# Kernel optimization log

Hardware: AMD Instinct MI355X
Metric: run time of the kernel (lower is better)

Reference implementation:

```python
import jax, jax.numpy as jnp
import numpy as np

V = 50000      # nodes
E = 800000     # edges (avg degree 16)
H = 128        # hidden_nf
EA = 2         # edge_attr dim after concat with radial dist
NL = 2         # n_layers
NORM = 100.0   # normalization_factor (agg_method='sum')
NORM_CONST = 1.0


def setup_inputs() -> dict:
    key = jax.random.key(0)
    ks = jax.random.split(key, 24)
    f32 = jnp.float32
    def rn(k, shp, s=0.02):
        return jax.random.normal(k, shp, dtype=f32) * s
    return {
        "h": jax.random.normal(ks[0], (V, H), f32),
        "x": jax.random.normal(ks[1], (V, 3), f32),
        "edge_index": jax.random.randint(ks[2], (2, E), 0, V),
        "edge_attr": jax.random.normal(ks[3], (E, 1), f32),
        # GCL params, stacked over NL layers
        "ew1": rn(ks[4], (NL, 2 * H + EA, H)), "eb1": jnp.zeros((NL, H), f32),
        "ew2": rn(ks[5], (NL, H, H)),          "eb2": jnp.zeros((NL, H), f32),
        "aw":  rn(ks[6], (NL, H, 1)),          "ab":  jnp.zeros((NL, 1), f32),
        "nw1": rn(ks[7], (NL, 2 * H, H)),      "nb1": jnp.zeros((NL, H), f32),
        "nw2": rn(ks[8], (NL, H, H)),          "nb2": jnp.zeros((NL, H), f32),
        # EquivariantUpdate coord_mlp params
        "cw1": rn(ks[9], (2 * H + EA, H)),     "cb1": jnp.zeros((H,), f32),
        "cw2": rn(ks[10], (H, H)),             "cb2": jnp.zeros((H,), f32),
        "cw3": rn(ks[11], (H, 1), 0.001),      # xavier gain=0.001, no bias
    }


def reference(h, x, edge_index, edge_attr,
              ew1, eb1, ew2, eb2, aw, ab, nw1, nb1, nw2, nb2,
              cw1, cb1, cw2, cb2, cw3):
    silu = jax.nn.silu
    row, col = edge_index[0], edge_index[1]

    # coord2diff
    coord_diff = x[row] - x[col]                               # [E,3]
    radial = jnp.sum(coord_diff ** 2, axis=1, keepdims=True)   # [E,1]
    norm = jnp.sqrt(radial + 1e-8)
    coord_diff = coord_diff / (norm + NORM_CONST)

    ea = jnp.concatenate([radial, edge_attr], axis=1)          # [E,EA]

    # n_layers GCL blocks with attention, agg_method='sum'
    for i in range(NL):
        inp = jnp.concatenate([h[row], h[col], ea], axis=1)    # [E,2H+EA]
        mij = silu(inp @ ew1[i] + eb1[i])
        mij = silu(mij @ ew2[i] + eb2[i])                      # [E,H]
        att = jax.nn.sigmoid(mij @ aw[i] + ab[i])              # [E,1]
        edge_feat = mij * att
        agg = jax.ops.segment_sum(edge_feat, row, num_segments=V) / NORM  # [V,H]
        t = jnp.concatenate([h, agg], axis=1)                  # [V,2H]
        t = silu(t @ nw1[i] + nb1[i])
        h = h + (t @ nw2[i] + nb2[i])

    # EquivariantUpdate (tanh=False)
    inp = jnp.concatenate([h[row], h[col], ea], axis=1)        # [E,2H+EA]
    t = silu(inp @ cw1 + cb1)
    t = silu(t @ cw2 + cb2)
    s = t @ cw3                                                # [E,1]
    trans = coord_diff * s                                     # [E,3]
    aggc = jax.ops.segment_sum(trans, row, num_segments=V) / NORM
    x = x + aggc
    return (h, x)
```

## Files before the change

### kernel.cpp

```cpp
#include <hip/hip_runtime.h>

#define V_N 50000
#define E_N 800000
#define H_N 128

typedef __bf16 bf16;
typedef bf16 bf16x4 __attribute__((ext_vector_type(4)));
typedef bf16 bf16x8 __attribute__((ext_vector_type(8)));
typedef float f32x4 __attribute__((ext_vector_type(4)));

#define PQ_STRIDE 512

__device__ __forceinline__ float silu_f(float x) {
    return x * __builtin_amdgcn_rcpf(1.0f + __expf(-x));
}
__device__ __forceinline__ float sigmoid_f(float x) {
    return __builtin_amdgcn_rcpf(1.0f + __expf(-x));
}

__global__ void k_weights(const float* __restrict__ ew1, const float* __restrict__ ew2,
                          const float* __restrict__ nw1, const float* __restrict__ nw2,
                          const float* __restrict__ cw1, const float* __restrict__ cw2,
                          const float* __restrict__ eb1, const float* __restrict__ cb1,
                          bf16* __restrict__ projT, bf16* __restrict__ ew2T,
                          bf16* __restrict__ nw1T, bf16* __restrict__ nw2T,
                          bf16* __restrict__ cprojT, bf16* __restrict__ cw2T,
                          float* __restrict__ biasPQ, float* __restrict__ biasCPQ) {
    int idx = blockIdx.x * 256 + threadIdx.x;
    if (idx < 65536) {
        int l = idx >> 15, rem = idx & 32767;
        int n = rem >> 7, k = rem & 127;
        const float* W = ew1 + l * 258 * 128;
        projT[idx] = (bf16)((n < 128) ? W[k * 128 + n] : W[(128 + k) * 128 + (n - 128)]);
    } else if (idx < 98304) {
        int r = idx - 65536;
        int l = r >> 14, rem = r & 16383;
        int n = rem >> 7, k = rem & 127;
        ew2T[r] = (bf16)(ew2[l * 16384 + k * 128 + n]);
    } else if (idx < 163840) {
        int r = idx - 98304;
        int l = r >> 15, rem = r & 32767;
        int n = rem >> 8, k = rem & 255;
        nw1T[r] = (bf16)(nw1[l * 32768 + k * 128 + n]);
    } else if (idx < 196608) {
        int r = idx - 163840;
        int l = r >> 14, rem = r & 16383;
        int n = rem >> 7, k = rem & 127;
        nw2T[r] = (bf16)(nw2[l * 16384 + k * 128 + n]);
    } else if (idx < 229376) {
        int r = idx - 196608;
        int n = r >> 7, k = r & 127;
        cprojT[r] = (bf16)((n < 128) ? cw1[k * 128 + n] : cw1[(128 + k) * 128 + (n - 128)]);
    } else if (idx < 245760) {
        int r = idx - 229376;
        int n = r >> 7, k = r & 127;
        cw2T[r] = (bf16)(cw2[k * 128 + n]);
    } else if (idx < 246272) {
        int r = idx - 245760;
        int l = r >> 8, c = r & 255;
        biasPQ[r] = (c < 128) ? eb1[l * 128 + c] : 0.0f;
    } else if (idx < 246528) {
        int c = idx - 246272;
        biasCPQ[c] = (c < 128) ? cb1[c] : 0.0f;
    }
}

__global__ void k_hist(const int* __restrict__ ei, int* __restrict__ cnt) {
    int e = blockIdx.x * 256 + threadIdx.x;
    if (e < E_N) atomicAdd(&cnt[ei[e]], 1);
}

__global__ __launch_bounds__(1024) void k_scan(const int* __restrict__ cnt,
                                               int* __restrict__ off) {
    __shared__ int wsum[16];
    __shared__ int wscan[16];
    __shared__ int carry_s;
    int tid = threadIdx.x;
    int lane = tid & 63, wid = tid >> 6;
    if (tid == 0) carry_s = 0;
    __syncthreads();
    for (int base = 0; base < V_N; base += 1024) {
        int carry = carry_s;
        int i = base + tid;
        int v = (i < V_N) ? cnt[i] : 0;
        int val = v;
#pragma unroll
        for (int d = 1; d < 64; d <<= 1) {
            int t = __shfl_up(val, d, 64);
            if (lane >= d) val += t;
        }
        if (lane == 63) wsum[wid] = val;
        __syncthreads();
        if (tid == 0) {
            int s = 0;
#pragma unroll
            for (int k = 0; k < 16; k++) { s += wsum[k]; wscan[k] = s; }
        }
        __syncthreads();
        int wbase = wid ? wscan[wid - 1] : 0;
        if (i < V_N) off[i] = carry + wbase + val - v;
        __syncthreads();
        if (tid == 0) carry_s = carry + wscan[15];
        __syncthreads();
    }
}

__global__ void k_scatter(const int* __restrict__ ei, int* __restrict__ off,
                          int* __restrict__ srow, int* __restrict__ scol,
                          int* __restrict__ perm) {
    int e = blockIdx.x * 256 + threadIdx.x;
    if (e >= E_N) return;
    int r = ei[e], c = ei[E_N + e];
    int p = atomicAdd(&off[r], 1);
    srow[p] = r;
    scol[p] = c;
    perm[p] = e;
}

__global__ void k_edgeprep2(const int* __restrict__ perm, const int* __restrict__ srow,
                            const int* __restrict__ scol, const float* __restrict__ x,
                            const float* __restrict__ eattr,
                            float* __restrict__ cd, float* __restrict__ ea2) {
    int p = blockIdx.x * 256 + threadIdx.x;
    if (p >= E_N) return;
    int e = perm[p];
    int r = srow[p], c = scol[p];
    float dx = x[r * 3 + 0] - x[c * 3 + 0];
    float dy = x[r * 3 + 1] - x[c * 3 + 1];
    float dz = x[r * 3 + 2] - x[c * 3 + 2];
    float rad = dx * dx + dy * dy + dz * dz;
    float inv = 1.0f / (sqrtf(rad + 1e-8f) + 1.0f);
    cd[p * 3 + 0] = dx * inv;
    cd[p * 3 + 1] = dy * inv;
    cd[p * 3 + 2] = dz * inv;
    ea2[p * 2 + 0] = rad;
    ea2[p * 2 + 1] = eattr[e];
}

__global__ __launch_bounds__(256) void k_node_gemm(
    const float* __restrict__ A1, const float* __restrict__ A2,
    const bf16* __restrict__ BT, const float* __restrict__ bias,
    const float* __restrict__ resid, float* __restrict__ C,
    int M, int K, int Ntot, int act, int opq) {
    __shared__ __align__(16) bf16 Asl[64][136];
    __shared__ __align__(16) bf16 Bsl[128][136];
    int tid = threadIdx.x;
    int m0 = blockIdx.x * 64;
    int n0 = blockIdx.y * 128;
    int lane = tid & 63, w = tid >> 6;
    int q = lane >> 4, l15 = lane & 15;

    f32x4 acc[8];
#pragma unroll
    for (int i = 0; i < 8; i++) acc[i] = (f32x4){0.f, 0.f, 0.f, 0.f};

    for (int kc = 0; kc < K; kc += 128) {
        const float* Asrc = (kc == 0) ? A1 : A2;
#pragma unroll
        for (int p = 0; p < 8; p++) {
            int e4 = (p * 256 + tid) * 4;
            int r = e4 >> 7, k = e4 & 127;
            float4 v = {0.f, 0.f, 0.f, 0.f};
            int row = m0 + r;
            if (row < M) v = *(const float4*)&Asrc[(size_t)row * 128 + k];
            bf16x4 b4 = {(bf16)v.x, (bf16)v.y, (bf16)v.z, (bf16)v.w};
            *(bf16x4*)&Asl[r][k] = b4;
        }
#pragma unroll
        for (int p = 0; p < 8; p++) {
            int e8 = (p * 256 + tid) * 8;
            int n = e8 >> 7, k = e8 & 127;
            bf16x8 v = *(const bf16x8*)&BT[(size_t)(n0 + n) * K + kc + k];
            *(bf16x8*)&Bsl[n][k] = v;
        }
        __syncthreads();
        int ar = w * 16 + l15;
#pragma unroll
        for (int kt = 0; kt < 4; kt++) {
            bf16x8 a = *(const bf16x8*)&Asl[ar][kt * 32 + q * 8];
#pragma unroll
            for (int nt = 0; nt < 8; nt++) {
                bf16x8 b = *(const bf16x8*)&Bsl[nt * 16 + l15][kt * 32 + q * 8];
                acc[nt] = __builtin_amdgcn_mfma_f32_16x16x32_bf16(a, b, acc[nt], 0, 0, 0);
            }
        }
        __syncthreads();
    }
#pragma unroll
    for (int nt = 0; nt < 8; nt++) {
        int col = n0 + nt * 16 + l15;
        float bv = bias ? bias[col] : 0.0f;
#pragma unroll
        for (int reg = 0; reg < 4; reg++) {
            int row = m0 + w * 16 + q * 4 + reg;
            if (row < M) {
                float v = acc[nt][reg] + bv;
                if (act) v = silu_f(v);
                if (resid) v += resid[(size_t)row * 128 + (col & 127)];
                if (opq) {
                    *(bf16*)((char*)C + (size_t)row * PQ_STRIDE + col * 2) = (bf16)v;
                } else {
                    C[(size_t)row * Ntot + col] = v;
                }
            }
        }
    }
}

__global__ __launch_bounds__(256) void k_node_mlp(
    float* __restrict__ A2,
    const bf16* __restrict__ B1T,
    const float* __restrict__ b1,
    const bf16* __restrict__ B2T,
    const float* __restrict__ b2,
    float* __restrict__ H,
    int M, int zeroA2,
    const bf16* __restrict__ PT,
    const float* __restrict__ pbias,
    char* __restrict__ PQout) {
    __shared__ __align__(16) bf16 Asl[64][136];
    __shared__ __align__(16) bf16 Bsl[128][136];
    int tid = threadIdx.x;
    int m0 = blockIdx.x * 64;
    int lane = tid & 63, w = tid >> 6;
    int q = lane >> 4, l15 = lane & 15;
    int ar = w * 16 + l15;

    f32x4 acc[8];
#pragma unroll
    for (int i = 0; i < 8; i++) acc[i] = (f32x4){0.f, 0.f, 0.f, 0.f};

    for (int kc = 0; kc < 256; kc += 128) {
        const float* Asrc = (kc == 0) ? H : A2;
#pragma unroll
        for (int p = 0; p < 8; p++) {
            int e4 = (p * 256 + tid) * 4;
            int r = e4 >> 7, k = e4 & 127;
            float4 v = {0.f, 0.f, 0.f, 0.f};
            int row = m0 + r;
            if (row < M) v = *(const float4*)&Asrc[(size_t)row * 128 + k];
            bf16x4 b4 = {(bf16)v.x, (bf16)v.y, (bf16)v.z, (bf16)v.w};
            *(bf16x4*)&Asl[r][k] = b4;
            if (kc == 128 && zeroA2 && row < M) {
                *(float4*)&A2[(size_t)row * 128 + k] = (float4){0.f, 0.f, 0.f, 0.f};
            }
        }
#pragma unroll
        for (int p = 0; p < 8; p++) {
            int e8 = (p * 256 + tid) * 8;
            int n = e8 >> 7, k = e8 & 127;
            bf16x8 v = *(const bf16x8*)&B1T[(size_t)n * 256 + kc + k];
            *(bf16x8*)&Bsl[n][k] = v;
        }
        __syncthreads();
#pragma unroll
        for (int kt = 0; kt < 4; kt++) {
            bf16x8 a = *(const bf16x8*)&Asl[ar][kt * 32 + q * 8];
#pragma unroll
            for (int nt = 0; nt < 8; nt++) {
                bf16x8 b = *(const bf16x8*)&Bsl[nt * 16 + l15][kt * 32 + q * 8];
                acc[nt] = __builtin_amdgcn_mfma_f32_16x16x32_bf16(a, b, acc[nt], 0, 0, 0);
            }
        }
        __syncthreads();
    }
#pragma unroll
    for (int nt = 0; nt < 8; nt++) {
        float bv = b1[nt * 16 + l15];
#pragma unroll
        for (int reg = 0; reg < 4; reg++) {
            int r = w * 16 + q * 4 + reg;
            Asl[r][nt * 16 + l15] = (bf16)silu_f(acc[nt][reg] + bv);
        }
    }
#pragma unroll
    for (int p = 0; p < 8; p++) {
        int e8 = (p * 256 + tid) * 8;
        int n = e8 >> 7, k = e8 & 127;
        *(bf16x8*)&Bsl[n][k] = *(const bf16x8*)&B2T[(size_t)n * 128 + k];
    }
    __syncthreads();
    f32x4 acc2[8];
#pragma unroll
    for (int i = 0; i < 8; i++) acc2[i] = (f32x4){0.f, 0.f, 0.f, 0.f};
#pragma unroll
    for (int kt = 0; kt < 4; kt++) {
        bf16x8 a = *(const bf16x8*)&Asl[ar][kt * 32 + q * 8];
#pragma unroll
        for (int nt = 0; nt < 8; nt++) {
            bf16x8 b = *(const bf16x8*)&Bsl[nt * 16 + l15][kt * 32 + q * 8];
            acc2[nt] = __builtin_amdgcn_mfma_f32_16x16x32_bf16(a, b, acc2[nt], 0, 0, 0);
        }
    }
#pragma unroll
    for (int nt = 0; nt < 8; nt++) {
        int col = nt * 16 + l15;
        float bv = b2[col];
#pragma unroll
        for (int reg = 0; reg < 4; reg++) {
            int row = m0 + w * 16 + q * 4 + reg;
            if (row < M) {
                float hv = H[(size_t)row * 128 + col] + acc2[nt][reg] + bv;
                H[(size_t)row * 128 + col] = hv;
                acc2[nt][reg] = hv;
            }
        }
    }
    __syncthreads();
#pragma unroll
    for (int nt = 0; nt < 8; nt++) {
#pragma unroll
        for (int reg = 0; reg < 4; reg++) {
            int r = w * 16 + q * 4 + reg;
            Asl[r][nt * 16 + l15] = (bf16)acc2[nt][reg];
        }
    }
    for (int half = 0; half < 2; half++) {
#pragma unroll
        for (int p = 0; p < 8; p++) {
            int e8 = (p * 256 + tid) * 8;
            int n = e8 >> 7, k = e8 & 127;
            *(bf16x8*)&Bsl[n][k] = *(const bf16x8*)&PT[(size_t)(half * 128 + n) * 128 + k];
        }
        __syncthreads();
        f32x4 accp[8];
#pragma unroll
        for (int i = 0; i < 8; i++) accp[i] = (f32x4){0.f, 0.f, 0.f, 0.f};
#pragma unroll
        for (int kt = 0; kt < 4; kt++) {
            bf16x8 a = *(const bf16x8*)&Asl[ar][kt * 32 + q * 8];
#pragma unroll
            for (int nt = 0; nt < 8; nt++) {
                bf16x8 b = *(const bf16x8*)&Bsl[nt * 16 + l15][kt * 32 + q * 8];
                accp[nt] = __builtin_amdgcn_mfma_f32_16x16x32_bf16(a, b, accp[nt], 0, 0, 0);
            }
        }
#pragma unroll
        for (int nt = 0; nt < 8; nt++) {
            int colg = half * 128 + nt * 16 + l15;
            float bv = pbias[colg];
#pragma unroll
            for (int reg = 0; reg < 4; reg++) {
                int row = m0 + w * 16 + q * 4 + reg;
                if (row < M) {
                    *(bf16*)(PQout + (size_t)row * PQ_STRIDE + colg * 2) =
                        (bf16)(accp[nt][reg] + bv);
                }
            }
        }
        __syncthreads();
    }
}

#define NTILES (E_N / 128)

__global__ __launch_bounds__(512, 4) void k_edge_gcl(
    const int* __restrict__ srow, const int* __restrict__ scol,
    const char* __restrict__ PQ,
    const float* __restrict__ ea2, const float* __restrict__ w1c,
    const bf16* __restrict__ ew2T,
    const float* __restrict__ eb2, const float* __restrict__ aw,
    const float* __restrict__ ab, float* __restrict__ agg) {
    __shared__ __align__(16) bf16 Asl[128][136];
    __shared__ __align__(16) bf16 Bsl[128][136];
    __shared__ int rows_s[128];
    __shared__ int cols_s[128];
    __shared__ float ra_s[128], aa_s[128];
    int tid = threadIdx.x;
    int lane = tid & 63, w = tid >> 6, q = lane >> 4, l15 = lane & 15;
    int j = (tid & 31) * 4;
    int eslot = tid >> 5;

#pragma unroll
    for (int p = 0; p < 4; p++) {
        int e8 = (p * 512 + tid) * 8;
        int n = e8 >> 7, k = e8 & 127;
        *(bf16x8*)&Bsl[n][k] = *(const bf16x8*)&ew2T[n * 128 + k];
    }
    float4 w0r = *(const float4*)&w1c[j];
    float4 w1r = *(const float4*)&w1c[128 + j];
    float b2v[8], awv[8];
#pragma unroll
    for (int nt = 0; nt < 8; nt++) {
        b2v[nt] = eb2[nt * 16 + l15];
        awv[nt] = aw[nt * 16 + l15];
    }
    float ab0 = ab[0];

    for (int t = blockIdx.x; t < NTILES; t += gridDim.x) {
        int e0 = t * 128;
        __syncthreads();
        if (tid < 128) {
            int e = e0 + tid;
            rows_s[tid] = srow[e];
            cols_s[tid] = scol[e];
            float2 rr = *(const float2*)&ea2[(size_t)e * 2];
            ra_s[tid] = rr.x;
            aa_s[tid] = rr.y;
        }
        __syncthreads();
        bf16x4 pb[8];
        bf16x4 qb[8];
#pragma unroll
        for (int p = 0; p < 8; p++) {
            int el = p * 16 + eslot;
            int row = rows_s[el], col = cols_s[el];
            pb[p] = *(const bf16x4*)(PQ + (size_t)row * PQ_STRIDE + j * 2);
            qb[p] = *(const bf16x4*)(PQ + (size_t)col * PQ_STRIDE + 256 + j * 2);
        }
#pragma unroll
        for (int p = 0; p < 8; p++) {
            int el = p * 16 + eslot;
            float ra = ra_s[el], aa = aa_s[el];
            float zx = (float)pb[p][0] + (float)qb[p][0];
            float zy = (float)pb[p][1] + (float)qb[p][1];
            float zz = (float)pb[p][2] + (float)qb[p][2];
            float zw = (float)pb[p][3] + (float)qb[p][3];
            zx = fmaf(aa, w1r.x, fmaf(ra, w0r.x, zx));
            zy = fmaf(aa, w1r.y, fmaf(ra, w0r.y, zy));
            zz = fmaf(aa, w1r.z, fmaf(ra, w0r.z, zz));
            zw = fmaf(aa, w1r.w, fmaf(ra, w0r.w, zw));
            bf16x4 b4 = {(bf16)silu_f(zx), (bf16)silu_f(zy),
                         (bf16)silu_f(zz), (bf16)silu_f(zw)};
            *(bf16x4*)&Asl[el][j] = b4;
        }
        __syncthreads();
        f32x4 acc[8];
#pragma unroll
        for (int i = 0; i < 8; i++) acc[i] = (f32x4){0.f, 0.f, 0.f, 0.f};
        int ar = w * 16 + l15;
#pragma unroll
        for (int kt = 0; kt < 4; kt++) {
            bf16x8 a = *(const bf16x8*)&Asl[ar][kt * 32 + q * 8];
#pragma unroll
            for (int nt = 0; nt < 8; nt++) {
                bf16x8 b = *(const bf16x8*)&Bsl[nt * 16 + l15][kt * 32 + q * 8];
                acc[nt] = __builtin_amdgcn_mfma_f32_16x16x32_bf16(a, b, acc[nt], 0, 0, 0);
            }
        }
        float partial[4] = {0.f, 0.f, 0.f, 0.f};
#pragma unroll
        for (int nt = 0; nt < 8; nt++) {
#pragma unroll
            for (int reg = 0; reg < 4; reg++) {
                float mv = silu_f(acc[nt][reg] + b2v[nt]);
                acc[nt][reg] = mv;
                partial[reg] += mv * awv[nt];
            }
        }
        float scale[4];
#pragma unroll
        for (int reg = 0; reg < 4; reg++) {
            float s = partial[reg];
            s += __shfl_xor(s, 1, 16);
            s += __shfl_xor(s, 2, 16);
            s += __shfl_xor(s, 4, 16);
            s += __shfl_xor(s, 8, 16);
            scale[reg] = sigmoid_f(s + ab0) * 0.01f;
        }
        __syncthreads();
#pragma unroll
        for (int reg = 0; reg < 4; reg++) {
            int er = w * 16 + q * 4 + reg;
            float sc = scale[reg];
#pragma unroll
            for (int nt = 0; nt < 8; nt++) {
                Asl[er][nt * 16 + l15] = (bf16)(acc[nt][reg] * sc);
            }
        }
        __syncthreads();
        int col = tid & 127, quarter = tid >> 7;
        int es = quarter * 32, ee = es + 32;
        float sum = 0.f;
        for (int el = es; el < ee; ++el) {
            sum += (float)Asl[el][col];
            int r = rows_s[el];
            int nxt = (el + 1 < ee) ? rows_s[el + 1] : -1;
            if (r != nxt) {
                atomicAdd(&agg[(size_t)r * 128 + col], sum);
                sum = 0.f;
            }
        }
    }
}

__global__ __launch_bounds__(512, 4) void k_edge_coord(
    const int* __restrict__ srow, const int* __restrict__ scol,
    const char* __restrict__ PQ,
    const float* __restrict__ ea2, const float* __restrict__ c1c,
    const bf16* __restrict__ cw2T,
    const float* __restrict__ cb2, const float* __restrict__ cw3,
    const float* __restrict__ cd, float* __restrict__ xagg) {
    __shared__ __align__(16) bf16 Asl[128][136];
    __shared__ __align__(16) bf16 Bsl[128][136];
    __shared__ int rows_s[128];
    __shared__ int cols_s[128];
    __shared__ float ra_s[128], aa_s[128];
    __shared__ float cds[384];
    __shared__ float Ssl[128];
    int tid = threadIdx.x;
    int lane = tid & 63, w = tid >> 6, q = lane >> 4, l15 = lane & 15;
    int j = (tid & 31) * 4;
    int eslot = tid >> 5;

#pragma unroll
    for (int p = 0; p < 4; p++) {
        int e8 = (p * 512 + tid) * 8;
        int n = e8 >> 7, k = e8 & 127;
        *(bf16x8*)&Bsl[n][k] = *(const bf16x8*)&cw2T[n * 128 + k];
    }
    float4 w0r = *(const float4*)&c1c[j];
    float4 w1r = *(const float4*)&c1c[128 + j];
    float b2v[8], w3v[8];
#pragma unroll
    for (int nt = 0; nt < 8; nt++) {
        b2v[nt] = cb2[nt * 16 + l15];
        w3v[nt] = cw3[nt * 16 + l15];
    }

    for (int t = blockIdx.x; t < NTILES; t += gridDim.x) {
        int e0 = t * 128;
        __syncthreads();
        if (tid < 128) {
            int e = e0 + tid;
            rows_s[tid] = srow[e];
            cols_s[tid] = scol[e];
            float2 rr = *(const float2*)&ea2[(size_t)e * 2];
            ra_s[tid] = rr.x;
            aa_s[tid] = rr.y;
        }
        if (tid < 384) cds[tid] = cd[(size_t)e0 * 3 + tid];
        __syncthreads();
        bf16x4 pb[8];
        bf16x4 qb[8];
#pragma unroll
        for (int p = 0; p < 8; p++) {
            int el = p * 16 + eslot;
            int row = rows_s[el], col = cols_s[el];
            pb[p] = *(const bf16x4*)(PQ + (size_t)row * PQ_STRIDE + j * 2);
            qb[p] = *(const bf16x4*)(PQ + (size_t)col * PQ_STRIDE + 256 + j * 2);
        }
#pragma unroll
        for (int p = 0; p < 8; p++) {
            int el = p * 16 + eslot;
            float ra = ra_s[el], aa = aa_s[el];
            float zx = (float)pb[p][0] + (float)qb[p][0];
            float zy = (float)pb[p][1] + (float)qb[p][1];
            float zz = (float)pb[p][2] + (float)qb[p][2];
            float zw = (float)pb[p][3] + (float)qb[p][3];
            zx = fmaf(aa, w1r.x, fmaf(ra, w0r.x, zx));
            zy = fmaf(aa, w1r.y, fmaf(ra, w0r.y, zy));
            zz = fmaf(aa, w1r.z, fmaf(ra, w0r.z, zz));
            zw = fmaf(aa, w1r.w, fmaf(ra, w0r.w, zw));
            bf16x4 b4 = {(bf16)silu_f(zx), (bf16)silu_f(zy),
                         (bf16)silu_f(zz), (bf16)silu_f(zw)};
            *(bf16x4*)&Asl[el][j] = b4;
        }
        __syncthreads();
        f32x4 acc[8];
#pragma unroll
        for (int i = 0; i < 8; i++) acc[i] = (f32x4){0.f, 0.f, 0.f, 0.f};
        int ar = w * 16 + l15;
#pragma unroll
        for (int kt = 0; kt < 4; kt++) {
            bf16x8 a = *(const bf16x8*)&Asl[ar][kt * 32 + q * 8];
#pragma unroll
            for (int nt = 0; nt < 8; nt++) {
                bf16x8 b = *(const bf16x8*)&Bsl[nt * 16 + l15][kt * 32 + q * 8];
                acc[nt] = __builtin_amdgcn_mfma_f32_16x16x32_bf16(a, b, acc[nt], 0, 0, 0);
            }
        }
        float partial[4] = {0.f, 0.f, 0.f, 0.f};
#pragma unroll
        for (int nt = 0; nt < 8; nt++) {
#pragma unroll
            for (int reg = 0; reg < 4; reg++) {
                float tv = silu_f(acc[nt][reg] + b2v[nt]);
                partial[reg] += tv * w3v[nt];
            }
        }
#pragma unroll
        for (int reg = 0; reg < 4; reg++) {
            float s = partial[reg];
            s += __shfl_xor(s, 1, 16);
            s += __shfl_xor(s, 2, 16);
            s += __shfl_xor(s, 4, 16);
            s += __shfl_xor(s, 8, 16);
            if (l15 == 0) Ssl[w * 16 + q * 4 + reg] = s * 0.01f;
        }
        __syncthreads();
        if (tid < 48) {
            int d = tid % 3, chunk = tid / 3;
            int es = chunk * 8, ee = es + 8;
            float sum = 0.f;
            for (int el = es; el < ee; ++el) {
                sum += cds[el * 3 + d] * Ssl[el];
                int r = rows_s[el];
                int nxt = (el + 1 < ee) ? rows_s[el + 1] : -1;
                if (r != nxt) {
                    atomicAdd(&xagg[(size_t)r * 3 + d], sum);
                    sum = 0.f;
                }
            }
        }
    }
}

__global__ void k_finalx(const float* __restrict__ x, const float* __restrict__ xagg,
                         float* __restrict__ outx) {
    int i = blockIdx.x * 256 + threadIdx.x;
    if (i < V_N * 3) outx[i] = x[i] + xagg[i];
}

extern "C" void kernel_launch(void* const* d_in, const int* in_sizes, int n_in,
                              void* d_out, int out_size, void* d_ws, size_t ws_size,
                              hipStream_t stream) {
    const float* h = (const float*)d_in[0];
    const float* x = (const float*)d_in[1];
    const int* ei = (const int*)d_in[2];
    const float* eattr = (const float*)d_in[3];
    const float* ew1 = (const float*)d_in[4];
    const float* eb1 = (const float*)d_in[5];
    const float* ew2 = (const float*)d_in[6];
    const float* eb2 = (const float*)d_in[7];
    const float* aw = (const float*)d_in[8];
    const float* ab = (const float*)d_in[9];
    const float* nw1 = (const float*)d_in[10];
    const float* nb1 = (const float*)d_in[11];
    const float* nw2 = (const float*)d_in[12];
    const float* nb2 = (const float*)d_in[13];
    const float* cw1 = (const float*)d_in[14];
    const float* cb1 = (const float*)d_in[15];
    const float* cw2 = (const float*)d_in[16];
    const float* cb2 = (const float*)d_in[17];
    const float* cw3 = (const float*)d_in[18];

    char* ws = (char*)d_ws;
    size_t off_b = 0;
    auto alloc = [&](size_t b) {
        size_t o = off_b;
        off_b += (b + 255) & ~(size_t)255;
        return o;
    };
    float* cd = (float*)(ws + alloc((size_t)E_N * 3 * 4));
    float* ea2 = (float*)(ws + alloc((size_t)E_N * 2 * 4));
    char* PQ = (char*)(ws + alloc((size_t)V_N * PQ_STRIDE));
    float* agg = (float*)(ws + alloc((size_t)V_N * 128 * 4));
    float* xagg = (float*)(ws + alloc((size_t)V_N * 3 * 4));
    bf16* projT = (bf16*)(ws + alloc(2 * 256 * 128 * 2));
    bf16* ew2T = (bf16*)(ws + alloc(2 * 128 * 128 * 2));
    bf16* nw1T = (bf16*)(ws + alloc(2 * 128 * 256 * 2));
    bf16* nw2T = (bf16*)(ws + alloc(2 * 128 * 128 * 2));
    bf16* cprojT = (bf16*)(ws + alloc(256 * 128 * 2));
    bf16* cw2T = (bf16*)(ws + alloc(128 * 128 * 2));
    float* biasPQ = (float*)(ws + alloc(2 * 256 * 4));
    float* biasCPQ = (float*)(ws + alloc(256 * 4));
    int* cnt = (int*)(ws + alloc((size_t)V_N * 4));
    int* offv = (int*)(ws + alloc((size_t)V_N * 4));
    int* srow = (int*)(ws + alloc((size_t)E_N * 4));
    int* scol = (int*)(ws + alloc((size_t)E_N * 4));
    int* perm = (int*)(ws + alloc((size_t)E_N * 4));

    float* outh = (float*)d_out;
    float* outx = outh + (size_t)V_N * 128;

    hipMemcpyAsync(outh, h, (size_t)V_N * 128 * 4, hipMemcpyDeviceToDevice, stream);
    k_weights<<<964, 256, 0, stream>>>(ew1, ew2, nw1, nw2, cw1, cw2, eb1, cb1,
                                       projT, ew2T, nw1T, nw2T, cprojT, cw2T,
                                       biasPQ, biasCPQ);
    hipMemsetAsync(cnt, 0, (size_t)V_N * 4, stream);
    k_hist<<<(E_N + 255) / 256, 256, 0, stream>>>(ei, cnt);
    k_scan<<<1, 1024, 0, stream>>>(cnt, offv);
    k_scatter<<<(E_N + 255) / 256, 256, 0, stream>>>(ei, offv, srow, scol, perm);
    k_edgeprep2<<<(E_N + 255) / 256, 256, 0, stream>>>(perm, srow, scol, x, eattr, cd, ea2);
    hipMemsetAsync(xagg, 0, (size_t)V_N * 3 * 4, stream);
    hipMemsetAsync(agg, 0, (size_t)V_N * 128 * 4, stream);

    int mblocks = (V_N + 63) / 64;
    dim3 gproj(mblocks, 2);
    k_node_gemm<<<gproj, 256, 0, stream>>>(outh, nullptr, projT, biasPQ, nullptr,
                                           (float*)PQ, V_N, 128, 256, 0, 1);
    k_edge_gcl<<<512, 512, 0, stream>>>(
        srow, scol, PQ, ea2, ew1 + 256 * 128,
        ew2T, eb2, aw, ab, agg);
    k_node_mlp<<<mblocks, 256, 0, stream>>>(agg, nw1T, nb1, nw2T, nb2, outh, V_N, 1,
                                            projT + 256 * 128, biasPQ + 256, PQ);
    k_edge_gcl<<<512, 512, 0, stream>>>(
        srow, scol, PQ, ea2, ew1 + (size_t)1 * 258 * 128 + 256 * 128,
        ew2T + 128 * 128, eb2 + 128, aw + 128, ab + 1, agg);
    k_node_mlp<<<mblocks, 256, 0, stream>>>(agg, nw1T + 128 * 256, nb1 + 128,
                                            nw2T + 128 * 128, nb2 + 128, outh, V_N, 0,
                                            cprojT, biasCPQ, PQ);
    k_edge_coord<<<512, 512, 0, stream>>>(srow, scol, PQ, ea2, cw1 + 256 * 128,
                                          cw2T, cb2, cw3, cd, xagg);
    k_finalx<<<(V_N * 3 + 255) / 256, 256, 0, stream>>>(x, xagg, outx);
}
```

Before: 771.7 us.

## Double-buffer edge metadata prefetch and transpose scatter staging in edge kernels

```diff
diff --git a/kernel.cpp b/kernel.cpp
--- a/kernel.cpp
+++ b/kernel.cpp
@@ -363,9 +363,10 @@
     const float* __restrict__ ab, float* __restrict__ agg) {
     __shared__ __align__(16) bf16 Asl[128][136];
     __shared__ __align__(16) bf16 Bsl[128][136];
-    __shared__ int rows_s[128];
-    __shared__ int cols_s[128];
-    __shared__ float ra_s[128], aa_s[128];
+    __shared__ int rows_s[2][128];
+    __shared__ int cols_s[2][128];
+    __shared__ float ra_s[2][128], aa_s[2][128];
+    bf16(*FslT)[40] = (bf16(*)[40])Asl;
     int tid = threadIdx.x;
     int lane = tid & 63, w = tid >> 6, q = lane >> 4, l15 = lane & 15;
     int j = (tid & 31) * 4;
@@ -387,31 +388,41 @@
     }
     float ab0 = ab[0];
 
-    for (int t = blockIdx.x; t < NTILES; t += gridDim.x) {
-        int e0 = t * 128;
-        __syncthreads();
-        if (tid < 128) {
-            int e = e0 + tid;
-            rows_s[tid] = srow[e];
-            cols_s[tid] = scol[e];
+    int t0 = blockIdx.x;
+    if (tid < 128) {
+        int e = t0 * 128 + tid;
+        rows_s[0][tid] = srow[e];
+        cols_s[0][tid] = scol[e];
+        float2 rr = *(const float2*)&ea2[(size_t)e * 2];
+        ra_s[0][tid] = rr.x;
+        aa_s[0][tid] = rr.y;
+    }
+
+    int b = 0;
+    for (int t = t0; t < NTILES; t += gridDim.x, b ^= 1) {
+        int tn = t + gridDim.x;
+        __syncthreads();
+        if (tn < NTILES && tid < 128) {
+            int e = tn * 128 + tid;
+            rows_s[b ^ 1][tid] = srow[e];
+            cols_s[b ^ 1][tid] = scol[e];
             float2 rr = *(const float2*)&ea2[(size_t)e * 2];
-            ra_s[tid] = rr.x;
-            aa_s[tid] = rr.y;
-        }
-        __syncthreads();
+            ra_s[b ^ 1][tid] = rr.x;
+            aa_s[b ^ 1][tid] = rr.y;
+        }
         bf16x4 pb[8];
         bf16x4 qb[8];
 #pragma unroll
         for (int p = 0; p < 8; p++) {
             int el = p * 16 + eslot;
-            int row = rows_s[el], col = cols_s[el];
+            int row = rows_s[b][el], col = cols_s[b][el];
             pb[p] = *(const bf16x4*)(PQ + (size_t)row * PQ_STRIDE + j * 2);
             qb[p] = *(const bf16x4*)(PQ + (size_t)col * PQ_STRIDE + 256 + j * 2);
         }
 #pragma unroll
         for (int p = 0; p < 8; p++) {
             int el = p * 16 + eslot;
-            float ra = ra_s[el], aa = aa_s[el];
+            float ra = ra_s[b][el], aa = aa_s[b][el];
             float zx = (float)pb[p][0] + (float)qb[p][0];
             float zy = (float)pb[p][1] + (float)qb[p][1];
             float zz = (float)pb[p][2] + (float)qb[p][2];
@@ -434,8 +445,8 @@
             bf16x8 a = *(const bf16x8*)&Asl[ar][kt * 32 + q * 8];
 #pragma unroll
             for (int nt = 0; nt < 8; nt++) {
-                bf16x8 b = *(const bf16x8*)&Bsl[nt * 16 + l15][kt * 32 + q * 8];
-                acc[nt] = __builtin_amdgcn_mfma_f32_16x16x32_bf16(a, b, acc[nt], 0, 0, 0);
+                bf16x8 bb = *(const bf16x8*)&Bsl[nt * 16 + l15][kt * 32 + q * 8];
+                acc[nt] = __builtin_amdgcn_mfma_f32_16x16x32_bf16(a, bb, acc[nt], 0, 0, 0);
             }
         }
         float partial[4] = {0.f, 0.f, 0.f, 0.f};
@@ -465,17 +476,23 @@
             float sc = scale[reg];
 #pragma unroll
             for (int nt = 0; nt < 8; nt++) {
-                Asl[er][nt * 16 + l15] = (bf16)(acc[nt][reg] * sc);
+                FslT[nt * 16 + l15][er] = (bf16)(acc[nt][reg] * sc);
             }
         }
         __syncthreads();
         int col = tid & 127, quarter = tid >> 7;
-        int es = quarter * 32, ee = es + 32;
+        int es = quarter * 32;
+        bf16x8 f[4];
+#pragma unroll
+        for (int k2 = 0; k2 < 4; k2++) {
+            f[k2] = *(const bf16x8*)&FslT[col][es + k2 * 8];
+        }
         float sum = 0.f;
-        for (int el = es; el < ee; ++el) {
-            sum += (float)Asl[el][col];
-            int r = rows_s[el];
-            int nxt = (el + 1 < ee) ? rows_s[el + 1] : -1;
+#pragma unroll
+        for (int el2 = 0; el2 < 32; ++el2) {
+            sum += (float)f[el2 >> 3][el2 & 7];
+            int r = rows_s[b][es + el2];
+            int nxt = (el2 < 31) ? rows_s[b][es + el2 + 1] : -1;
             if (r != nxt) {
                 atomicAdd(&agg[(size_t)r * 128 + col], sum);
                 sum = 0.f;
@@ -493,10 +510,10 @@
     const float* __restrict__ cd, float* __restrict__ xagg) {
     __shared__ __align__(16) bf16 Asl[128][136];
     __shared__ __align__(16) bf16 Bsl[128][136];
-    __shared__ int rows_s[128];
-    __shared__ int cols_s[128];
-    __shared__ float ra_s[128], aa_s[128];
-    __shared__ float cds[384];
+    __shared__ int rows_s[2][128];
+    __shared__ int cols_s[2][128];
+    __shared__ float ra_s[2][128], aa_s[2][128];
+    __shared__ float cds[2][384];
     __shared__ float Ssl[128];
     int tid = threadIdx.x;
     int lane = tid & 63, w = tid >> 6, q = lane >> 4, l15 = lane & 15;
@@ -518,32 +535,45 @@
         w3v[nt] = cw3[nt * 16 + l15];
     }
 
-    for (int t = blockIdx.x; t < NTILES; t += gridDim.x) {
-        int e0 = t * 128;
-        __syncthreads();
-        if (tid < 128) {
-            int e = e0 + tid;
-            rows_s[tid] = srow[e];
-            cols_s[tid] = scol[e];
-            float2 rr = *(const float2*)&ea2[(size_t)e * 2];
-            ra_s[tid] = rr.x;
-            aa_s[tid] = rr.y;
-        }
-        if (tid < 384) cds[tid] = cd[(size_t)e0 * 3 + tid];
-        __syncthreads();
+    int t0 = blockIdx.x;
+    if (tid < 128) {
+        int e = t0 * 128 + tid;
+        rows_s[0][tid] = srow[e];
+        cols_s[0][tid] = scol[e];
+        float2 rr = *(const float2*)&ea2[(size_t)e * 2];
+        ra_s[0][tid] = rr.x;
+        aa_s[0][tid] = rr.y;
+    }
+    if (tid < 384) cds[0][tid] = cd[(size_t)t0 * 384 + tid];
+
+    int b = 0;
+    for (int t = t0; t < NTILES; t += gridDim.x, b ^= 1) {
+        int tn = t + gridDim.x;
+        __syncthreads();
+        if (tn < NTILES) {
+            if (tid < 128) {
+                int e = tn * 128 + tid;
+                rows_s[b ^ 1][tid] = srow[e];
+                cols_s[b ^ 1][tid] = scol[e];
+                float2 rr = *(const float2*)&ea2[(size_t)e * 2];
+                ra_s[b ^ 1][tid] = rr.x;
+                aa_s[b ^ 1][tid] = rr.y;
+            }
+            if (tid < 384) cds[b ^ 1][tid] = cd[(size_t)tn * 384 + tid];
+        }
         bf16x4 pb[8];
         bf16x4 qb[8];
 #pragma unroll
         for (int p = 0; p < 8; p++) {
             int el = p * 16 + eslot;
-            int row = rows_s[el], col = cols_s[el];
+            int row = rows_s[b][el], col = cols_s[b][el];
             pb[p] = *(const bf16x4*)(PQ + (size_t)row * PQ_STRIDE + j * 2);
             qb[p] = *(const bf16x4*)(PQ + (size_t)col * PQ_STRIDE + 256 + j * 2);
         }
 #pragma unroll
         for (int p = 0; p < 8; p++) {
             int el = p * 16 + eslot;
-            float ra = ra_s[el], aa = aa_s[el];
+            float ra = ra_s[b][el], aa = aa_s[b][el];
             float zx = (float)pb[p][0] + (float)qb[p][0];
             float zy = (float)pb[p][1] + (float)qb[p][1];
             float zz = (float)pb[p][2] + (float)qb[p][2];
@@ -566,8 +596,8 @@
             bf16x8 a = *(const bf16x8*)&Asl[ar][kt * 32 + q * 8];
 #pragma unroll
             for (int nt = 0; nt < 8; nt++) {
-                bf16x8 b = *(const bf16x8*)&Bsl[nt * 16 + l15][kt * 32 + q * 8];
-                acc[nt] = __builtin_amdgcn_mfma_f32_16x16x32_bf16(a, b, acc[nt], 0, 0, 0);
+                bf16x8 bb = *(const bf16x8*)&Bsl[nt * 16 + l15][kt * 32 + q * 8];
+                acc[nt] = __builtin_amdgcn_mfma_f32_16x16x32_bf16(a, bb, acc[nt], 0, 0, 0);
             }
         }
         float partial[4] = {0.f, 0.f, 0.f, 0.f};
@@ -594,9 +624,9 @@
             int es = chunk * 8, ee = es + 8;
             float sum = 0.f;
             for (int el = es; el < ee; ++el) {
-                sum += cds[el * 3 + d] * Ssl[el];
-                int r = rows_s[el];
-                int nxt = (el + 1 < ee) ? rows_s[el + 1] : -1;
+                sum += cds[b][el * 3 + d] * Ssl[el];
+                int r = rows_s[b][el];
+                int nxt = (el + 1 < ee) ? rows_s[b][el + 1] : -1;
                 if (r != nxt) {
                     atomicAdd(&xagg[(size_t)r * 3 + d], sum);
                     sum = 0.f;
```

New measurement: 765.7 us. No clear change (-0.8%).
